# Optimization experiments

Measured on AMD Instinct MI355X. Metric: run time of the kernel, lower is better.

Reference implementation:

```python
import jax, jax.numpy as jnp
import numpy as np
from jax import lax

B_, L_, IN, H, LYR = 8, 512, 64, 512, 4
ED, N, DC, DTR = 2 * H, 16, 4, 32  # d_inner, d_state, d_conv, dt_rank (mamba.py defaults)


def setup_inputs() -> dict:
    key = jax.random.key(0)
    ks = iter(jax.random.split(key, 24))
    def nrm(shape, s=0.02):
        return jax.random.normal(next(ks), shape, jnp.float32) * s
    A_log = jnp.tile(jnp.log(jnp.arange(1, N + 1, dtype=jnp.float32))[None, None, :], (LYR, ED, 1))
    return {
        "x": jax.random.normal(next(ks), (B_, L_, IN), jnp.float32),
        "w_in": nrm((H, IN)), "b_in": jnp.zeros((H,), jnp.float32),
        "ln1_w": jnp.ones((H,), jnp.float32), "ln1_b": jnp.zeros((H,), jnp.float32),
        "norm_w": jnp.ones((LYR, H), jnp.float32),
        "in_proj_w": nrm((LYR, 2 * ED, H)),
        "conv_w": nrm((LYR, ED, DC)), "conv_b": jnp.zeros((LYR, ED), jnp.float32),
        "x_proj_w": nrm((LYR, DTR + 2 * N, ED)),
        "dt_proj_w": nrm((LYR, ED, DTR)), "dt_proj_b": nrm((LYR, ED), 0.1),
        "A_log": A_log, "D": jnp.ones((LYR, ED), jnp.float32),
        "out_proj_w": nrm((LYR, H, ED)),
        "w_ref": nrm((H, H)), "b_ref": jnp.zeros((H,), jnp.float32),
        "ln2_w": jnp.ones((H,), jnp.float32), "ln2_b": jnp.zeros((H,), jnp.float32),
        "w_o1": nrm((H // 2, H)), "b_o1": jnp.zeros((H // 2,), jnp.float32),
        "w_o2": nrm((1, H // 2)), "b_o2": jnp.zeros((1,), jnp.float32),
    }


def _ln(x, w, b):
    mu = x.mean(-1, keepdims=True)
    xc = x - mu
    return xc * lax.rsqrt((xc * xc).mean(-1, keepdims=True) + 1e-5) * w + b


def _rms(x, w):
    return x * lax.rsqrt((x * x).mean(-1, keepdims=True) + 1e-5) * w


def _scan(dA, dBu, C):
    # dA, dBu: (B, L, ED, N); C: (B, L, N) -> y: (B, L, ED)
    def step(h, t):
        dA_t, dBu_t, c_t = t
        h = dA_t * h + dBu_t
        return h, jnp.einsum('ben,bn->be', h, c_t)
    h0 = jnp.zeros((dA.shape[0], ED, N), dA.dtype)
    _, ys = lax.scan(step, h0, (dA.swapaxes(0, 1), dBu.swapaxes(0, 1), C.swapaxes(0, 1)))
    return ys.swapaxes(0, 1)


def _mixer(x, in_w, cw, cb, xp_w, dt_w, dt_b, A_log, D, out_w):
    xz = x @ in_w.T                               # (B, L, 2*ED)
    xc, z = jnp.split(xz, 2, axis=-1)
    # depthwise causal conv1d, kernel DC, left-pad DC-1
    xt = lax.conv_general_dilated(xc.swapaxes(1, 2), cw[:, None, :], (1,), [(DC - 1, 0)],
                                  dimension_numbers=('NCH', 'OIH', 'NCH'), feature_group_count=ED)
    u = jax.nn.silu(xt.swapaxes(1, 2) + cb)       # (B, L, ED)
    dbc = u @ xp_w.T                              # (B, L, DTR + 2N)
    delta = jax.nn.softplus(dbc[..., :DTR] @ dt_w.T + dt_b)   # (B, L, ED)
    Bm, Cm = dbc[..., DTR:DTR + N], dbc[..., DTR + N:]
    A = -jnp.exp(A_log)                           # (ED, N)
    dA = jnp.exp(delta[..., None] * A)            # (B, L, ED, N)
    dBu = delta[..., None] * Bm[:, :, None, :] * u[..., None]
    y = _scan(dA, dBu, Cm) + D * u
    return (y * jax.nn.silu(z)) @ out_w.T


def reference(x, w_in, b_in, ln1_w, ln1_b, norm_w, in_proj_w, conv_w, conv_b, x_proj_w,
              dt_proj_w, dt_proj_b, A_log, D, out_proj_w, w_ref, b_ref, ln2_w, ln2_b,
              w_o1, b_o1, w_o2, b_o2):
    h = jax.nn.gelu(_ln(x @ w_in.T + b_in, ln1_w, ln1_b), approximate=False)
    hm = h
    for l in range(LYR):  # residual Mamba blocks (pre-RMSNorm)
        hm = hm + _mixer(_rms(hm, norm_w[l]), in_proj_w[l], conv_w[l], conv_b[l], x_proj_w[l],
                         dt_proj_w[l], dt_proj_b[l], A_log[l], D[l], out_proj_w[l])
    h = h + hm
    h = jax.nn.gelu(_ln(h @ w_ref.T + b_ref, ln2_w, ln2_b), approximate=False)  # dropout=eval
    h = jax.nn.gelu(h @ w_o1.T + b_o1, approximate=False)
    y = jax.nn.sigmoid(h @ w_o2.T + b_o2)
    return y[..., 0]
```

## Files before the change

### kernel.cpp

```cpp
#include <hip/hip_runtime.h>
#include <math.h>


#define BL 4096
#define H_ 512
#define ED_ 1024
#define N_ 16
#define DTR_ 32
#define CCH 16
#define TCH 32
#define L2E 1.44269504088896340736f

typedef unsigned short u16;
typedef unsigned int u32;
typedef __attribute__((ext_vector_type(8))) short short8;
typedef __attribute__((ext_vector_type(4))) float f32x4;

__device__ __forceinline__ float fexp2_(float x){ return __builtin_amdgcn_exp2f(x); }
__device__ __forceinline__ float geluf_(float x){ return 0.5f*x*(1.f+erff(x*0.70710678118654752f)); }
__device__ __forceinline__ float softplusf_(float x){ return (x>20.f)? x : log1pf(expf(x)); }
__device__ __forceinline__ float siluf_(float x){ return x/(1.f+fexp2_(-L2E*x)); }

__device__ __forceinline__ void split_bf16(float x, u16& hi, u16& lo){
  u32 u = __float_as_uint(x);
  u32 r = (u + 0x7fffu + ((u>>16)&1u)) >> 16;
  hi = (u16)r;
  float hf = __uint_as_float(r<<16);
  float rem = x - hf;
  u32 v = __float_as_uint(rem);
  lo = (u16)((v + 0x7fffu + ((v>>16)&1u)) >> 16);
}

__device__ __forceinline__ float block_reduce_sum(float v, float* sm){
  #pragma unroll
  for (int o=32;o>0;o>>=1) v += __shfl_down(v,o,64);
  if ((threadIdx.x&63)==0) sm[threadIdx.x>>6]=v;
  __syncthreads();
  float r = sm[0]+sm[1]+sm[2]+sm[3];
  __syncthreads();
  return r;
}

#define GLOAD_LDS16(g, l) __builtin_amdgcn_global_load_lds( \
    (const __attribute__((address_space(1))) u32*)(g), \
    (__attribute__((address_space(3))) u32*)(l), 16, 0, 0)

#define LDSBUF ((128+64)*64)
template<int ACT, int HAS_BIAS, int HAS_RES>
__device__ __forceinline__ void stage_tile(
  const u16* __restrict__ A, int lda, const u16* __restrict__ B, int ldb,
  int m0, int n0, int K, int kt, int tid, u16* lbase)
{
  #pragma unroll
  for (int i=0;i<4;i++){
    int c = tid + i*256;
    int r = c>>3, s = c&7;
    int j = s ^ (r&7);
    int col = (j<4) ? (kt + (j<<3)) : (K + kt + ((j-4)<<3));
    GLOAD_LDS16(A + (size_t)(m0+r)*lda + col, lbase + c*8);
  }
  #pragma unroll
  for (int i=0;i<2;i++){
    int c = tid + i*256;
    int r = c>>3, s = c&7;
    int j = s ^ (r&7);
    int col = (j<4) ? (kt + (j<<3)) : (K + kt + ((j-4)<<3));
    GLOAD_LDS16(B + (size_t)(n0+r)*ldb + col, lbase + 128*64 + c*8);
  }
}

template<int ACT, int HAS_BIAS, int HAS_RES>
__global__ __launch_bounds__(256) void mfma_gemm(
  const u16* __restrict__ A, int lda,
  const u16* __restrict__ B, int ldb,
  float* __restrict__ C, int ldc,
  const float* __restrict__ bias,
  const float* __restrict__ res,
  int K)
{
  __shared__ u16 lds[2*LDSBUF];
  int tid = threadIdx.x;
  int lane = tid & 63, w = tid >> 6;
  int wr = w >> 1, wc = w & 1;
  int nbx = gridDim.x;
  int nb  = nbx * gridDim.y;
  int lid = blockIdx.y*nbx + blockIdx.x;
  int cpx = nb >> 3;
  int swz = (lid & 7)*cpx + (lid >> 3);
  int m0 = (swz / nbx)*128, n0 = (swz % nbx)*64;

  f32x4 acc[4][2] = {};
  const int NK = K >> 5;
  stage_tile<ACT,HAS_BIAS,HAS_RES>(A,lda,B,ldb,m0,n0,K,0,tid,&lds[0]);
  __syncthreads();
  int cur = 0;
  for (int t=0; t<NK; t++){
    if (t+1 < NK)
      stage_tile<ACT,HAS_BIAS,HAS_RES>(A,lda,B,ldb,m0,n0,K,(t+1)<<5,tid,&lds[(cur^1)*LDSBUF]);
    const char* lb = (const char*)&lds[cur*LDSBUF];
    int kb = (lane>>4)<<4;
    short8 ah[4], al[4], bh[2], bl[2];
    #pragma unroll
    for (int fr=0; fr<4; fr++){
      int row = wr*64 + fr*16 + (lane&15);
      int sw = (row&7)<<4;
      ah[fr] = *(const short8*)(lb + row*128 + (kb ^ sw));
      al[fr] = *(const short8*)(lb + row*128 + ((64+kb) ^ sw));
    }
    #pragma unroll
    for (int fc=0; fc<2; fc++){
      int row = wc*32 + fc*16 + (lane&15);
      int sw = (row&7)<<4;
      bh[fc] = *(const short8*)(lb + 128*128 + row*128 + (kb ^ sw));
      bl[fc] = *(const short8*)(lb + 128*128 + row*128 + ((64+kb) ^ sw));
    }
    #pragma unroll
    for (int fr=0; fr<4; fr++)
      #pragma unroll
      for (int fc=0; fc<2; fc++)
        acc[fr][fc] = __builtin_amdgcn_mfma_f32_16x16x32_bf16(ah[fr], bh[fc], acc[fr][fc], 0,0,0);
    #pragma unroll
    for (int fr=0; fr<4; fr++)
      #pragma unroll
      for (int fc=0; fc<2; fc++)
        acc[fr][fc] = __builtin_amdgcn_mfma_f32_16x16x32_bf16(al[fr], bh[fc], acc[fr][fc], 0,0,0);
    #pragma unroll
    for (int fr=0; fr<4; fr++)
      #pragma unroll
      for (int fc=0; fc<2; fc++)
        acc[fr][fc] = __builtin_amdgcn_mfma_f32_16x16x32_bf16(ah[fr], bl[fc], acc[fr][fc], 0,0,0);
    __syncthreads();
    cur ^= 1;
  }
  #pragma unroll
  for (int fr=0; fr<4; fr++){
    #pragma unroll
    for (int fc=0; fc<2; fc++){
      #pragma unroll
      for (int j=0;j<4;j++){
        int m = m0 + wr*64 + fr*16 + (lane>>4)*4 + j;
        int n = n0 + wc*32 + fc*16 + (lane&15);
        float v = acc[fr][fc][j];
        if (HAS_BIAS) v += bias[n];
        if (ACT==1) v = geluf_(v);
        if (HAS_RES) v += res[(size_t)m*ldc + n];
        C[(size_t)m*ldc + n] = v;
      }
    }
  }
}

__global__ __launch_bounds__(256) void wconv_kernel(
  const float* __restrict__ in, u16* __restrict__ out, int kbits)
{
  size_t i = (size_t)blockIdx.x*256 + threadIdx.x;
  int K = 1<<kbits;
  size_t n = i >> kbits;
  int k = (int)(i & (size_t)(K-1));
  u16 hi, lo; split_bf16(in[i], hi, lo);
  size_t ob = n << (kbits+1);
  out[ob + k] = hi; out[ob + K + k] = lo;
}

template<int ACT, int HAS_BIAS, int HAS_RES, int SPLITK=1>
__global__ __launch_bounds__(256) void gemm_bt(
  const float* __restrict__ A, int lda,
  const float* __restrict__ B, int ldb,
  float* __restrict__ C, int ldc,
  const float* __restrict__ bias,
  const float* __restrict__ res,
  int K)
{
  __shared__ float As[16][65];
  __shared__ float Bs[16][65];
  int tid = threadIdx.x;
  int tx = tid & 15, ty = tid >> 4;
  int m0 = blockIdx.y*64, n0 = blockIdx.x*64;
  int k0 = 0, k1 = K;
  if (SPLITK>1){ int Ks = K/SPLITK; k0 = blockIdx.z*Ks; k1 = k0 + Ks; }
  float acc[4][4] = {};
  for (int kt=k0; kt<k1; kt+=16){
    #pragma unroll
    for (int i=0;i<4;i++){
      int idx = tid + i*256;
      int r = idx>>4, c = idx&15;
      As[c][r] = A[(size_t)(m0+r)*lda + kt + c];
      Bs[c][r] = B[(size_t)(n0+r)*ldb + kt + c];
    }
    __syncthreads();
    #pragma unroll
    for (int k=0;k<16;k++){
      float a[4],b[4];
      #pragma unroll
      for (int i=0;i<4;i++) a[i]=As[k][ty*4+i];
      #pragma unroll
      for (int j=0;j<4;j++) b[j]=Bs[k][tx*4+j];
      #pragma unroll
      for (int i=0;i<4;i++)
        #pragma unroll
        for (int j=0;j<4;j++)
          acc[i][j] = fmaf(a[i], b[j], acc[i][j]);
    }
    __syncthreads();
  }
  #pragma unroll
  for (int i=0;i<4;i++){
    int m = m0 + ty*4 + i;
    #pragma unroll
    for (int j=0;j<4;j++){
      int n = n0 + tx*4 + j;
      float v = acc[i][j];
      if (SPLITK>1){
        atomicAdd(&C[(size_t)m*ldc + n], v);
      } else {
        if (HAS_BIAS) v += bias[n];
        if (ACT==1) v = geluf_(v);
        else if (ACT==2) v = softplusf_(v);
        if (HAS_RES) v += res[(size_t)m*ldc + n];
        C[(size_t)m*ldc + n] = v;
      }
    }
  }
}

__global__ __launch_bounds__(256) void dt_flat_kernel(
  const float* __restrict__ dbc, const float* __restrict__ dt_w,
  const float* __restrict__ dt_b, float* __restrict__ delta)
{
  int e  = (blockIdx.x & 3)*256 + threadIdx.x;
  int mg = blockIdx.x >> 2;
  f32x4 w[8];
  const f32x4* wp = (const f32x4*)(dt_w + (size_t)e*DTR_);
  #pragma unroll
  for (int q=0;q<8;q++) w[q] = wp[q];
  float bias = dt_b[e];
  #pragma unroll
  for (int i=0;i<4;i++){
    int m = mg*4 + i;
    const f32x4* dp = (const f32x4*)(dbc + (size_t)m*64);
    float s = 0.f;
    #pragma unroll
    for (int q=0;q<8;q++){
      f32x4 d = dp[q];
      #pragma unroll
      for (int j=0;j<4;j++) s = fmaf(d[j], w[q][j], s);
    }
    delta[(size_t)m*ED_ + e] = softplusf_(s + bias);
  }
}

__global__ __launch_bounds__(256) void zero_kernel(float* __restrict__ p){
  p[(size_t)blockIdx.x*256 + threadIdx.x] = 0.f;
}

__global__ __launch_bounds__(256) void ln_gelu_kernel(
  const float* __restrict__ in, const float* __restrict__ w, const float* __restrict__ b,
  float* __restrict__ out1, float* __restrict__ out2)
{
  __shared__ float sm[4];
  size_t row = blockIdx.x;
  const float* xr = in + row*H_;
  int t = threadIdx.x;
  float x0 = xr[t], x1 = xr[t+256];
  float mu = block_reduce_sum(x0+x1, sm) * (1.f/512.f);
  float c0 = x0-mu, c1 = x1-mu;
  float var = block_reduce_sum(c0*c0+c1*c1, sm) * (1.f/512.f);
  float rs = rsqrtf(var + 1e-5f);
  float y0 = geluf_(c0*rs*w[t]     + b[t]);
  float y1 = geluf_(c1*rs*w[t+256] + b[t+256]);
  out1[row*H_+t] = y0; out1[row*H_+t+256] = y1;
  if (out2){ out2[row*H_+t] = y0; out2[row*H_+t+256] = y1; }
}

__global__ __launch_bounds__(256) void ln_gelu_b3_kernel(
  const float* __restrict__ in, const float* __restrict__ w, const float* __restrict__ b,
  u16* __restrict__ out)
{
  __shared__ float sm[4];
  size_t row = blockIdx.x;
  const float* xr = in + row*H_;
  int t = threadIdx.x;
  float x0 = xr[t], x1 = xr[t+256];
  float mu = block_reduce_sum(x0+x1, sm) * (1.f/512.f);
  float c0 = x0-mu, c1 = x1-mu;
  float var = block_reduce_sum(c0*c0+c1*c1, sm) * (1.f/512.f);
  float rs = rsqrtf(var + 1e-5f);
  float y0 = geluf_(c0*rs*w[t]     + b[t]);
  float y1 = geluf_(c1*rs*w[t+256] + b[t+256]);
  u16 hi,lo;
  split_bf16(y0,hi,lo); out[row*1024 + t]     = hi; out[row*1024 + 512 + t]     = lo;
  split_bf16(y1,hi,lo); out[row*1024 + t+256] = hi; out[row*1024 + 512 + t+256] = lo;
}

__global__ __launch_bounds__(256) void rms_b3_kernel(
  const float* __restrict__ in, const float* __restrict__ w, u16* __restrict__ out)
{
  __shared__ float sm[4];
  size_t row = blockIdx.x;
  const float* xr = in + row*H_;
  int t = threadIdx.x;
  float x0 = xr[t], x1 = xr[t+256];
  float ss = block_reduce_sum(x0*x0+x1*x1, sm) * (1.f/512.f);
  float rs = rsqrtf(ss + 1e-5f);
  float y0 = x0*rs*w[t], y1 = x1*rs*w[t+256];
  u16 hi,lo;
  split_bf16(y0,hi,lo); out[row*1024 + t]     = hi; out[row*1024 + 512 + t]     = lo;
  split_bf16(y1,hi,lo); out[row*1024 + t+256] = hi; out[row*1024 + 512 + t+256] = lo;
}

__global__ __launch_bounds__(256) void add_b3_kernel(
  const float* __restrict__ a, const float* __restrict__ b, u16* __restrict__ out)
{
  size_t i = (size_t)blockIdx.x*256 + threadIdx.x;
  float v = a[i] + b[i];
  size_t r = i >> 9, c = i & 511;
  u16 hi,lo; split_bf16(v,hi,lo);
  out[r*1024 + c] = hi; out[r*1024 + 512 + c] = lo;
}

__global__ __launch_bounds__(256) void conv_silu_kernel(
  const float* __restrict__ xz, const float* __restrict__ cw, const float* __restrict__ cb,
  float* __restrict__ u)
{
  int token = blockIdx.x;
  int e = blockIdx.y*256 + threadIdx.x;
  int b = token >> 9, t = token & 511;
  float acc = cb[e];
  #pragma unroll
  for (int k=0;k<4;k++){
    int tt = t - 3 + k;
    if (tt >= 0) acc = fmaf(cw[e*4+k], xz[((size_t)((b<<9)|tt))*2048 + e], acc);
  }
  u[(size_t)token*ED_ + e] = siluf_(acc);
}


__global__ __launch_bounds__(256) void scan_pass1(
  const float* __restrict__ delta, const float* __restrict__ u,
  const float* __restrict__ dbc, const float* __restrict__ A_log,
  float* __restrict__ dts_out, float* __restrict__ Sb)
{
  int gid = blockIdx.x*256 + threadIdx.x;
  int e = gid & 1023;
  int c = (gid >> 10) & (CCH-1);
  int b = gid >> 14;
  int p = (b<<10) | e;
  float al2[16];
  {
    const f32x4* ar = (const f32x4*)(A_log + e*16);
    #pragma unroll
    for (int q=0;q<4;q++){
      f32x4 av = ar[q];
      #pragma unroll
      for (int j=0;j<4;j++) al2[q*4+j] = -fexp2_(av[j]*L2E)*L2E;
    }
  }
  int tokbase = (b<<9) + c*TCH;
  const float* dptr = delta + (size_t)tokbase*ED_ + e;
  const float* uptr = u     + (size_t)tokbase*ED_ + e;
  const f32x4* bc   = (const f32x4*)(dbc + (size_t)tokbase*64 + 32);
  float S[16];
  #pragma unroll
  for (int n=0;n<16;n++) S[n]=0.f;
  float dts = 0.f;
  float dt = dptr[0], ut = uptr[0];
  f32x4 Bv[4];
  #pragma unroll
  for (int q=0;q<4;q++) Bv[q] = bc[q];
  #pragma unroll 4
  for (int t=0;t<TCH;t++){
    int tn = (t+1 < TCH) ? t+1 : t;
    float ndt = dptr[(size_t)tn*ED_];
    float nut = uptr[(size_t)tn*ED_];
    f32x4 nBv[4];
    #pragma unroll
    for (int q=0;q<4;q++) nBv[q] = bc[tn*16+q];
    float du = dt*ut;
    dts += dt;
    #pragma unroll
    for (int q=0;q<4;q++)
      #pragma unroll
      for (int j=0;j<4;j++){
        int n = q*4+j;
        float da = fexp2_(dt*al2[n]);
        S[n] = fmaf(da, S[n], du*Bv[q][j]);
      }
    dt = ndt; ut = nut;
    #pragma unroll
    for (int q=0;q<4;q++) Bv[q] = nBv[q];
  }
  f32x4* sp = (f32x4*)(Sb + ((size_t)(c*8192 + p))*16);
  #pragma unroll
  for (int q=0;q<4;q++){
    f32x4 sv; sv[0]=S[q*4]; sv[1]=S[q*4+1]; sv[2]=S[q*4+2]; sv[3]=S[q*4+3];
    sp[q] = sv;
  }
  dts_out[c*8192 + p] = dts;
}

__global__ __launch_bounds__(256) void scan_pass2(
  const float* __restrict__ dts, float* __restrict__ Sb,
  const float* __restrict__ A_log)
{
  int i = blockIdx.x*256 + threadIdx.x;
  int n = i & 15;
  int p = i >> 4;
  int e = p & 1023;
  float al2 = -fexp2_(A_log[e*16+n]*L2E)*L2E;
  float h = 0.f;
  #pragma unroll
  for (int c=0;c<CCH;c++){
    size_t off = (size_t)c*(8192*16) + i;
    float S = Sb[off];
    Sb[off] = h;
    float P = fexp2_(al2 * dts[c*8192 + p]);
    h = fmaf(P, h, S);
  }
}

__global__ __launch_bounds__(256) void scan_pass3(
  const float* __restrict__ delta, const float* __restrict__ u,
  const float* __restrict__ dbc, const float* __restrict__ xz,
  const float* __restrict__ A_log, const float* __restrict__ D,
  const float* __restrict__ hin,
  u16* __restrict__ g3)
{
  int gid = blockIdx.x*256 + threadIdx.x;
  int e = gid & 1023;
  int c = (gid >> 10) & (CCH-1);
  int b = gid >> 14;
  int p = (b<<10) | e;
  float al2[16];
  {
    const f32x4* ar = (const f32x4*)(A_log + e*16);
    #pragma unroll
    for (int q=0;q<4;q++){
      f32x4 av = ar[q];
      #pragma unroll
      for (int j=0;j<4;j++) al2[q*4+j] = -fexp2_(av[j]*L2E)*L2E;
    }
  }
  float h[16];
  {
    const f32x4* hp = (const f32x4*)(hin + ((size_t)(c*8192 + p))*16);
    #pragma unroll
    for (int q=0;q<4;q++){
      f32x4 hv = hp[q];
      #pragma unroll
      for (int j=0;j<4;j++) h[q*4+j] = hv[j];
    }
  }
  float de = D[e];
  int tokbase = (b<<9) + c*TCH;
  const float* dptr = delta + (size_t)tokbase*ED_ + e;
  const float* uptr = u     + (size_t)tokbase*ED_ + e;
  const f32x4* bc   = (const f32x4*)(dbc + (size_t)tokbase*64 + 32);
  const float* zptr = xz + (size_t)tokbase*2048 + 1024 + e;
  u16* gp = g3 + (size_t)tokbase*4096 + e;
  float dt = dptr[0], ut = uptr[0], zt = zptr[0];
  f32x4 Bv[4], Cv[4];
  #pragma unroll
  for (int q=0;q<4;q++){ Bv[q] = bc[q]; Cv[q] = bc[4+q]; }
  #pragma unroll 4
  for (int t=0;t<TCH;t++){
    int tn = (t+1 < TCH) ? t+1 : t;
    float ndt = dptr[(size_t)tn*ED_];
    float nut = uptr[(size_t)tn*ED_];
    float nzt = zptr[(size_t)tn*2048];
    f32x4 nBv[4], nCv[4];
    #pragma unroll
    for (int q=0;q<4;q++){ nBv[q] = bc[tn*16+q]; nCv[q] = bc[tn*16+4+q]; }
    float du = dt*ut;
    float yq[4] = {0.f,0.f,0.f,0.f};
    #pragma unroll
    for (int q=0;q<4;q++)
      #pragma unroll
      for (int j=0;j<4;j++){
        int n = q*4+j;
        float da = fexp2_(dt*al2[n]);
        h[n] = fmaf(da, h[n], du*Bv[q][j]);
        yq[q] = fmaf(h[n], Cv[q][j], yq[q]);
      }
    float y = (yq[0]+yq[1]) + (yq[2]+yq[3]);
    float gv = (y + de*ut) * siluf_(zt);
    u16 hi,lo; split_bf16(gv,hi,lo);
    gp[(size_t)t*4096] = hi; gp[(size_t)t*4096 + 1024] = lo;
    dt = ndt; ut = nut; zt = nzt;
    #pragma unroll
    for (int q=0;q<4;q++){ Bv[q] = nBv[q]; Cv[q] = nCv[q]; }
  }
}

__global__ __launch_bounds__(64) void head_kernel(
  const float* __restrict__ t2, const float* __restrict__ w, const float* __restrict__ b,
  float* __restrict__ out)
{
  int token = blockIdx.x;
  int lane = threadIdx.x;
  float s = 0.f;
  #pragma unroll
  for (int i=0;i<4;i++){
    int c = lane + i*64;
    s = fmaf(t2[(size_t)token*256 + c], w[c], s);
  }
  #pragma unroll
  for (int o=32;o>0;o>>=1) s += __shfl_down(s,o,64);
  if (lane==0) out[token] = 1.f/(1.f+expf(-(s + b[0])));
}

extern "C" void kernel_launch(void* const* d_in, const int* in_sizes, int n_in,
                              void* d_out, int out_size, void* d_ws, size_t ws_size,
                              hipStream_t stream) {
  const float* x         = (const float*)d_in[0];
  const float* w_in      = (const float*)d_in[1];
  const float* b_in      = (const float*)d_in[2];
  const float* ln1_w     = (const float*)d_in[3];
  const float* ln1_b     = (const float*)d_in[4];
  const float* norm_w    = (const float*)d_in[5];
  const float* in_proj_w = (const float*)d_in[6];
  const float* conv_w    = (const float*)d_in[7];
  const float* conv_b    = (const float*)d_in[8];
  const float* x_proj_w  = (const float*)d_in[9];
  const float* dt_proj_w = (const float*)d_in[10];
  const float* dt_proj_b = (const float*)d_in[11];
  const float* A_log     = (const float*)d_in[12];
  const float* Dp        = (const float*)d_in[13];
  const float* out_proj_w= (const float*)d_in[14];
  const float* w_ref     = (const float*)d_in[15];
  const float* b_ref     = (const float*)d_in[16];
  const float* ln2_w     = (const float*)d_in[17];
  const float* ln2_b     = (const float*)d_in[18];
  const float* w_o1      = (const float*)d_in[19];
  const float* b_o1      = (const float*)d_in[20];
  const float* w_o2      = (const float*)d_in[21];
  const float* b_o2      = (const float*)d_in[22];
  float* out = (float*)d_out;

  float* ws   = (float*)d_ws;
  float* h0   = ws;
  float* hm   = h0   + (size_t)BL*H_;
  float* t512 = hm   + (size_t)BL*H_;
  float* xz   = t512 + (size_t)BL*H_;
  float* u    = xz   + (size_t)BL*2048;
  float* dbc  = u    + (size_t)BL*ED_;
  float* delta= dbc  + (size_t)BL*64;
  float* t2   = delta+ (size_t)BL*ED_;

  u16* a3u  = (u16*)t512;
  u16* wb3u = (u16*)t2;
  u16* wt3u = (u16*)hm;
  u16* g3u  = (u16*)xz;
  float* Sb   = t512;
  float* dts  = t2;

  gemm_bt<0,1,0><<<dim3(8,64),256,0,stream>>>(x,64, w_in,64, t512,H_, b_in,nullptr, 64);
  ln_gelu_kernel<<<BL,256,0,stream>>>(t512, ln1_w, ln1_b, h0, hm);

  for (int l=0;l<4;l++){
    rms_b3_kernel<<<BL,256,0,stream>>>(hm, norm_w + l*H_, a3u);
    wconv_kernel<<<2048*512/256,256,0,stream>>>(in_proj_w + (size_t)l*2048*H_, wb3u, 9);
    mfma_gemm<0,0,0><<<dim3(32,32),256,0,stream>>>(a3u,1024, wb3u,1024, xz,2048, nullptr,nullptr, 512);
    conv_silu_kernel<<<dim3(BL,4),256,0,stream>>>(xz, conv_w + l*ED_*4, conv_b + l*ED_, u);
    zero_kernel<<<BL*64/256,256,0,stream>>>(dbc);
    gemm_bt<0,0,0,4><<<dim3(1,64,4),256,0,stream>>>(u,ED_, x_proj_w + (size_t)l*64*ED_, ED_, dbc,64, nullptr,nullptr, ED_);
    dt_flat_kernel<<<BL,256,0,stream>>>(dbc, dt_proj_w + (size_t)l*ED_*DTR_, dt_proj_b + l*ED_, delta);
    scan_pass1<<<8192*CCH/256,256,0,stream>>>(delta, u, dbc, A_log + (size_t)l*ED_*N_, dts, Sb);
    scan_pass2<<<8192*16/256,256,0,stream>>>(dts, Sb, A_log + (size_t)l*ED_*N_);
    scan_pass3<<<8192*CCH/256,256,0,stream>>>(delta, u, dbc, xz, A_log + (size_t)l*ED_*N_, Dp + l*ED_, Sb, g3u);
    wconv_kernel<<<512*1024/256,256,0,stream>>>(out_proj_w + (size_t)l*H_*ED_, wb3u, 10);
    mfma_gemm<0,0,1><<<dim3(8,32),256,0,stream>>>(g3u,4096, wb3u,2048, hm,512, nullptr, hm, 1024);
  }

  add_b3_kernel<<<BL*H_/256,256,0,stream>>>(h0, hm, a3u);
  wconv_kernel<<<512*512/256,256,0,stream>>>(w_ref, wt3u, 9);
  mfma_gemm<0,1,0><<<dim3(8,32),256,0,stream>>>(a3u,1024, wt3u,1024, u,512, b_ref, nullptr, 512);
  ln_gelu_b3_kernel<<<BL,256,0,stream>>>(u, ln2_w, ln2_b, a3u);
  wconv_kernel<<<256*512/256,256,0,stream>>>(w_o1, wt3u, 9);
  mfma_gemm<1,1,0><<<dim3(4,32),256,0,stream>>>(a3u,1024, wt3u,1024, t2,256, b_o1, nullptr, 512);
  head_kernel<<<BL,64,0,stream>>>(t2, w_o2, b_o2, out);
}
```

Measured before the change: 887.3 us.

## Replace split-K atomic x_proj GEMM with dedicated in-block K-split reduction kernel

The x_proj projection (4096x64 output, K=1024) previously ran as a zero-fill kernel followed by a split-K tiled GEMM that accumulated its partial sums with global atomics over only 256 blocks. It now runs as one dedicated kernel of 1024 blocks. Each block handles 4 rows, splits K across 16 thread groups using vectorized float4 loads, and reduces the partials in shared memory before a plain store. This removes a launch, the zeroing pass and the atomics, and raises parallelism. The cost is that the weight is re-read from cache by every block with less data reuse.

```diff
diff --git a/kernel.cpp b/kernel.cpp
--- a/kernel.cpp
+++ b/kernel.cpp
@@ -162,7 +162,7 @@
   out[ob + k] = hi; out[ob + K + k] = lo;
 }
 
-template<int ACT, int HAS_BIAS, int HAS_RES, int SPLITK=1>
+template<int ACT, int HAS_BIAS, int HAS_RES>
 __global__ __launch_bounds__(256) void gemm_bt(
   const float* __restrict__ A, int lda,
   const float* __restrict__ B, int ldb,
@@ -176,10 +176,8 @@
   int tid = threadIdx.x;
   int tx = tid & 15, ty = tid >> 4;
   int m0 = blockIdx.y*64, n0 = blockIdx.x*64;
-  int k0 = 0, k1 = K;
-  if (SPLITK>1){ int Ks = K/SPLITK; k0 = blockIdx.z*Ks; k1 = k0 + Ks; }
   float acc[4][4] = {};
-  for (int kt=k0; kt<k1; kt+=16){
+  for (int kt=0; kt<K; kt+=16){
     #pragma unroll
     for (int i=0;i<4;i++){
       int idx = tid + i*256;
@@ -210,17 +208,57 @@
     for (int j=0;j<4;j++){
       int n = n0 + tx*4 + j;
       float v = acc[i][j];
-      if (SPLITK>1){
-        atomicAdd(&C[(size_t)m*ldc + n], v);
-      } else {
-        if (HAS_BIAS) v += bias[n];
-        if (ACT==1) v = geluf_(v);
-        else if (ACT==2) v = softplusf_(v);
-        if (HAS_RES) v += res[(size_t)m*ldc + n];
-        C[(size_t)m*ldc + n] = v;
+      if (HAS_BIAS) v += bias[n];
+      if (ACT==1) v = geluf_(v);
+      else if (ACT==2) v = softplusf_(v);
+      if (HAS_RES) v += res[(size_t)m*ldc + n];
+      C[(size_t)m*ldc + n] = v;
+    }
+  }
+}
+
+__global__ __launch_bounds__(256) void xproj_kernel(
+  const float* __restrict__ u, const float* __restrict__ xw,
+  float* __restrict__ dbc)
+{
+  __shared__ float red[16*257];
+  int t = threadIdx.x;
+  int n4 = t & 15, i = t >> 4;
+  int m0 = blockIdx.x * 4;
+  float acc[4][4] = {};
+  const f32x4* up[4];
+  #pragma unroll
+  for (int m=0;m<4;m++) up[m] = (const f32x4*)(u + (size_t)(m0+m)*1024 + i*64);
+  const f32x4* wp[4];
+  #pragma unroll
+  for (int j=0;j<4;j++) wp[j] = (const f32x4*)(xw + (size_t)(n4+16*j)*1024 + i*64);
+  #pragma unroll 4
+  for (int q=0;q<16;q++){
+    f32x4 w4[4], u4[4];
+    #pragma unroll
+    for (int j=0;j<4;j++) w4[j] = wp[j][q];
+    #pragma unroll
+    for (int m=0;m<4;m++) u4[m] = up[m][q];
+    #pragma unroll
+    for (int m=0;m<4;m++)
+      #pragma unroll
+      for (int j=0;j<4;j++){
+        acc[m][j] = fmaf(u4[m][0], w4[j][0], acc[m][j]);
+        acc[m][j] = fmaf(u4[m][1], w4[j][1], acc[m][j]);
+        acc[m][j] = fmaf(u4[m][2], w4[j][2], acc[m][j]);
+        acc[m][j] = fmaf(u4[m][3], w4[j][3], acc[m][j]);
       }
-    }
-  }
+  }
+  #pragma unroll
+  for (int m=0;m<4;m++)
+    #pragma unroll
+    for (int j=0;j<4;j++)
+      red[i*257 + m*64 + n4 + 16*j] = acc[m][j];
+  __syncthreads();
+  float s = 0.f;
+  #pragma unroll
+  for (int i2=0;i2<16;i2++) s += red[i2*257 + t];
+  dbc[(size_t)(m0 + (t>>6))*64 + (t&63)] = s;
 }
 
 __global__ __launch_bounds__(256) void dt_flat_kernel(
@@ -247,10 +285,6 @@
     }
     delta[(size_t)m*ED_ + e] = softplusf_(s + bias);
   }
-}
-
-__global__ __launch_bounds__(256) void zero_kernel(float* __restrict__ p){
-  p[(size_t)blockIdx.x*256 + threadIdx.x] = 0.f;
 }
 
 __global__ __launch_bounds__(256) void ln_gelu_kernel(
@@ -561,8 +595,7 @@
     wconv_kernel<<<2048*512/256,256,0,stream>>>(in_proj_w + (size_t)l*2048*H_, wb3u, 9);
     mfma_gemm<0,0,0><<<dim3(32,32),256,0,stream>>>(a3u,1024, wb3u,1024, xz,2048, nullptr,nullptr, 512);
     conv_silu_kernel<<<dim3(BL,4),256,0,stream>>>(xz, conv_w + l*ED_*4, conv_b + l*ED_, u);
-    zero_kernel<<<BL*64/256,256,0,stream>>>(dbc);
-    gemm_bt<0,0,0,4><<<dim3(1,64,4),256,0,stream>>>(u,ED_, x_proj_w + (size_t)l*64*ED_, ED_, dbc,64, nullptr,nullptr, ED_);
+    xproj_kernel<<<BL/4,256,0,stream>>>(u, x_proj_w + (size_t)l*64*ED_, dbc);
     dt_flat_kernel<<<BL,256,0,stream>>>(dbc, dt_proj_w + (size_t)l*ED_*DTR_, dt_proj_b + l*ED_, delta);
     scan_pass1<<<8192*CCH/256,256,0,stream>>>(delta, u, dbc, A_log + (size_t)l*ED_*N_, dts, Sb);
     scan_pass2<<<8192*16/256,256,0,stream>>>(dts, Sb, A_log + (size_t)l*ED_*N_);
```

Result: slower. 923.2 us (+4.1%).
